# Performance work log

Hardware: AMD Instinct MI355X
Metric: run time of the kernel (lower is better)

The kernel has to match this reference:

```python
import jax, jax.numpy as jnp
import numpy as np


def setup_inputs() -> dict:
    key = jax.random.key(0)
    # coeffs_tensor: stacked/padded wavelet coefficients [B, F, T]
    coeffs = jax.random.normal(key, (16, 256, 8192), dtype=jnp.float32)
    return {"coeffs": coeffs}


def reference(coeffs) -> jnp.ndarray:
    B, F, T = coeffs.shape
    # torch.angle on a real tensor -> 0 for x>=0, pi for x<0; jnp.angle matches.
    phase = jnp.angle(coeffs)
    inst_freq = jnp.diff(phase, axis=-1)
    inst_freq = jnp.pad(inst_freq, ((0, 0), (0, 0), (0, 1)))  # F.pad(..., (0,1))
    freq_adjusted = jnp.clip(inst_freq, -1.0, 1.0)  # [B,F,T]
    # k = (f + freq_adjusted).long(); .long() truncates toward zero, as does astype(int32)
    f_idx = jnp.arange(F, dtype=coeffs.dtype)[None, :, None]
    k = jnp.clip((f_idx + freq_adjusted).astype(jnp.int32), 0, F - 1)  # [B,F,T]
    # Fused scatter-add over all (b, f, t): sst[b, k[b,f,t], t] += coeffs[b, f, t]
    b_idx = jnp.arange(B)[:, None, None]
    t_idx = jnp.arange(T)[None, None, :]
    sst = jnp.zeros_like(coeffs).at[b_idx, k, t_idx].add(coeffs)
    return sst
```

## Files before the change

kernel.cpp:

```cpp
#include <hip/hip_runtime.h>

typedef float f32x4 __attribute__((ext_vector_type(4)));

#define BB 16
#define FF 256
#define TT 8192
#define F_CHUNK 8
#define ROWS (F_CHUNK + 2)
#define THREADS 256

__device__ __forceinline__ int sgn_bit(float x) {
    return (int)(__float_as_uint(x) >> 31);
}

__global__ __launch_bounds__(THREADS, 6) void sst_kernel(const float* __restrict__ in,
                                                         float* __restrict__ out) {
    const int t  = blockIdx.x * (THREADS * 4) + threadIdx.x * 4;
    const int fs = blockIdx.y * F_CHUNK;
    const int b  = blockIdx.z;

    const float* src = in  + (size_t)b * FF * TT + t;
    float*       dst = out + (size_t)b * FF * TT + t;

    const bool tail = (t + 4 >= TT);
    const int  eoff = tail ? 3 : 4;

    f32x4    v[ROWS];
    float    e[ROWS];
    unsigned pk[ROWS];

    #pragma unroll
    for (int i = 0; i < ROWS; ++i) {
        int f = fs - 1 + i;
        f = f < 0 ? 0 : (f > FF - 1 ? FF - 1 : f);
        const float* p = src + (size_t)f * TT;
        v[i] = *reinterpret_cast<const f32x4*>(p);
        e[i] = p[eoff];
    }

    __builtin_amdgcn_sched_barrier(0);

    #pragma unroll
    for (int i = 0; i < ROWS; ++i) {
        const int f = fs - 1 + i;
        const bool oob = (f < 0) | (f > FF - 1);
        const int s0 = sgn_bit(v[i][0]), s1 = sgn_bit(v[i][1]),
                  s2 = sgn_bit(v[i][2]), s3 = sgn_bit(v[i][3]), s4 = sgn_bit(e[i]);
        const int a0 = s1 - s0 + 1;
        const int a1 = s2 - s1 + 1;
        const int a2 = s3 - s2 + 1;
        const int a3 = tail ? 1 : (s4 - s3 + 1);
        pk[i] = oob ? 0x55u : (unsigned)(a0 | (a1 << 2) | (a2 << 4) | (a3 << 6));
    }

    #pragma unroll
    for (int i = 1; i <= F_CHUNK; ++i) {
        const int g = fs + (i - 1);
        const bool isFirst = (g == 0);
        const bool isLast  = (g == FF - 1);

        const unsigned pp = pk[i - 1], pc = pk[i], pn = pk[i + 1];
        const f32x4    vp = v[i - 1],  vc = v[i],  vn = v[i + 1];

        f32x4 r;
        {
            const unsigned cp = pp & 3u, cc = pc & 3u, cn = pn & 3u;
            const bool bc = (cc == 1u) || (isFirst && cc == 0u) || (isLast && cc == 2u);
            r[0] = ((cp == 2u) ? vp[0] : 0.f) + (bc ? vc[0] : 0.f) + ((cn == 0u) ? vn[0] : 0.f);
        }
        {
            const unsigned cp = (pp >> 2) & 3u, cc = (pc >> 2) & 3u, cn = (pn >> 2) & 3u;
            const bool bc = (cc == 1u) || (isFirst && cc == 0u) || (isLast && cc == 2u);
            r[1] = ((cp == 2u) ? vp[1] : 0.f) + (bc ? vc[1] : 0.f) + ((cn == 0u) ? vn[1] : 0.f);
        }
        {
            const unsigned cp = (pp >> 4) & 3u, cc = (pc >> 4) & 3u, cn = (pn >> 4) & 3u;
            const bool bc = (cc == 1u) || (isFirst && cc == 0u) || (isLast && cc == 2u);
            r[2] = ((cp == 2u) ? vp[2] : 0.f) + (bc ? vc[2] : 0.f) + ((cn == 0u) ? vn[2] : 0.f);
        }
        {
            const unsigned cp = (pp >> 6) & 3u, cc = (pc >> 6) & 3u, cn = (pn >> 6) & 3u;
            const bool bc = (cc == 1u) || (isFirst && cc == 0u) || (isLast && cc == 2u);
            r[3] = ((cp == 2u) ? vp[3] : 0.f) + (bc ? vc[3] : 0.f) + ((cn == 0u) ? vn[3] : 0.f);
        }

        __builtin_nontemporal_store(r, reinterpret_cast<f32x4*>(dst + (size_t)g * TT));
    }
}

extern "C" void kernel_launch(void* const* d_in, const int* in_sizes, int n_in,
                              void* d_out, int out_size, void* d_ws, size_t ws_size,
                              hipStream_t stream) {
    const float* in  = (const float*)d_in[0];
    float*       out = (float*)d_out;
    dim3 grid(TT / (THREADS * 4), FF / F_CHUNK, BB);
    sst_kernel<<<grid, THREADS, 0, stream>>>(in, out);
}
```

Before: 236.7 us.

## Loop over time tiles per block with double-buffered global-to-LDS async loads

Each block now owns an F-chunk for one batch and walks all time tiles, staging rows into LDS through global_load_lds DMA with two buffers so the next tiles load while the current one computes. Tile-boundary columns, whose next element lies in the following tile, are patched in a separate epilogue that rereads global memory. This is meant to hide load latency and remove the per-block extra edge loads. The cost is far fewer blocks (512) that each run long, hand-tuned vmcnt counts that must exactly match the DMA ordering, and an epilogue with scattered scalar accesses.

```diff
diff --git a/kernel.cpp b/kernel.cpp
--- a/kernel.cpp
+++ b/kernel.cpp
@@ -8,83 +8,150 @@
 #define F_CHUNK 8
 #define ROWS (F_CHUNK + 2)
 #define THREADS 256
+#define TBLK (THREADS * 4)
+#define TILES (TT / TBLK)
+#define LROW 1024
+
+__device__ __forceinline__ void dma16(const float* g, float* l) {
+    __builtin_amdgcn_global_load_lds(
+        (const __attribute__((address_space(1))) unsigned int*)g,
+        (__attribute__((address_space(3))) unsigned int*)l,
+        16, 0, 0);
+}
 
 __device__ __forceinline__ int sgn_bit(float x) {
     return (int)(__float_as_uint(x) >> 31);
 }
 
-__global__ __launch_bounds__(THREADS, 6) void sst_kernel(const float* __restrict__ in,
-                                                         float* __restrict__ out) {
-    const int t  = blockIdx.x * (THREADS * 4) + threadIdx.x * 4;
-    const int fs = blockIdx.y * F_CHUNK;
-    const int b  = blockIdx.z;
+__global__ __launch_bounds__(THREADS) void sst_kernel(const float* __restrict__ in,
+                                                      float* __restrict__ out) {
+    __shared__ float sm[2][ROWS][LROW];
 
-    const float* src = in  + (size_t)b * FF * TT + t;
-    float*       dst = out + (size_t)b * FF * TT + t;
+    const int tid  = threadIdx.x;
+    const int wid  = tid >> 6;
+    const int tid4 = tid * 4;
+    const int fs   = blockIdx.x * F_CHUNK;
+    const int b    = blockIdx.y;
 
-    const bool tail = (t + 4 >= TT);
-    const int  eoff = tail ? 3 : 4;
+    const float* srcR = in  + (size_t)b * FF * TT;
+    float*       dstR = out + (size_t)b * FF * TT;
 
-    f32x4    v[ROWS];
-    float    e[ROWS];
-    unsigned pk[ROWS];
+    const int eidx = (tid4 + 4 > LROW - 1) ? (LROW - 1) : (tid4 + 4);
+
+#define STAGE(tt, bb_) do {                                                        \
+        _Pragma("unroll")                                                          \
+        for (int i_ = 0; i_ < ROWS; ++i_) {                                        \
+            int f_ = fs - 1 + i_;                                                  \
+            f_ = f_ < 0 ? 0 : (f_ > FF - 1 ? FF - 1 : f_);                         \
+            dma16(srcR + (size_t)f_ * TT + (tt) * TBLK + tid4,                     \
+                  &sm[bb_][i_][wid * 256]);                                        \
+        }                                                                          \
+    } while (0)
+
+    STAGE(0, 0);
+    STAGE(1, 1);
 
     #pragma unroll
-    for (int i = 0; i < ROWS; ++i) {
-        int f = fs - 1 + i;
-        f = f < 0 ? 0 : (f > FF - 1 ? FF - 1 : f);
-        const float* p = src + (size_t)f * TT;
-        v[i] = *reinterpret_cast<const f32x4*>(p);
-        e[i] = p[eoff];
-    }
+    for (int k = 0; k < TILES; ++k) {
+        if (k == 0)              asm volatile("s_waitcnt vmcnt(10)" ::: "memory");
+        else if (k == TILES - 1) asm volatile("s_waitcnt vmcnt(16)" ::: "memory");
+        else                     asm volatile("s_waitcnt vmcnt(18)" ::: "memory");
+        __builtin_amdgcn_sched_barrier(0);
+        __builtin_amdgcn_s_barrier();
+        asm volatile("" ::: "memory");
 
-    __builtin_amdgcn_sched_barrier(0);
+        const int bb = k & 1;
 
-    #pragma unroll
-    for (int i = 0; i < ROWS; ++i) {
-        const int f = fs - 1 + i;
-        const bool oob = (f < 0) | (f > FF - 1);
-        const int s0 = sgn_bit(v[i][0]), s1 = sgn_bit(v[i][1]),
-                  s2 = sgn_bit(v[i][2]), s3 = sgn_bit(v[i][3]), s4 = sgn_bit(e[i]);
-        const int a0 = s1 - s0 + 1;
-        const int a1 = s2 - s1 + 1;
-        const int a2 = s3 - s2 + 1;
-        const int a3 = tail ? 1 : (s4 - s3 + 1);
-        pk[i] = oob ? 0x55u : (unsigned)(a0 | (a1 << 2) | (a2 << 4) | (a3 << 6));
-    }
+        f32x4 v[ROWS];
+        float ee[ROWS];
+        #pragma unroll
+        for (int i = 0; i < ROWS; ++i) {
+            v[i]  = *reinterpret_cast<const f32x4*>(&sm[bb][i][tid4]);
+            ee[i] = sm[bb][i][eidx];
+        }
+        asm volatile("s_waitcnt lgkmcnt(0)" ::: "memory");
+        __builtin_amdgcn_sched_barrier(0);
+        __builtin_amdgcn_s_barrier();
+        asm volatile("" ::: "memory");
 
-    #pragma unroll
-    for (int i = 1; i <= F_CHUNK; ++i) {
-        const int g = fs + (i - 1);
-        const bool isFirst = (g == 0);
-        const bool isLast  = (g == FF - 1);
+        if (k + 2 < TILES) STAGE(k + 2, bb);
 
-        const unsigned pp = pk[i - 1], pc = pk[i], pn = pk[i + 1];
-        const f32x4    vp = v[i - 1],  vc = v[i],  vn = v[i + 1];
-
-        f32x4 r;
-        {
-            const unsigned cp = pp & 3u, cc = pc & 3u, cn = pn & 3u;
-            const bool bc = (cc == 1u) || (isFirst && cc == 0u) || (isLast && cc == 2u);
-            r[0] = ((cp == 2u) ? vp[0] : 0.f) + (bc ? vc[0] : 0.f) + ((cn == 0u) ? vn[0] : 0.f);
-        }
-        {
-            const unsigned cp = (pp >> 2) & 3u, cc = (pc >> 2) & 3u, cn = (pn >> 2) & 3u;
-            const bool bc = (cc == 1u) || (isFirst && cc == 0u) || (isLast && cc == 2u);
-            r[1] = ((cp == 2u) ? vp[1] : 0.f) + (bc ? vc[1] : 0.f) + ((cn == 0u) ? vn[1] : 0.f);
-        }
-        {
-            const unsigned cp = (pp >> 4) & 3u, cc = (pc >> 4) & 3u, cn = (pn >> 4) & 3u;
-            const bool bc = (cc == 1u) || (isFirst && cc == 0u) || (isLast && cc == 2u);
-            r[2] = ((cp == 2u) ? vp[2] : 0.f) + (bc ? vc[2] : 0.f) + ((cn == 0u) ? vn[2] : 0.f);
-        }
-        {
-            const unsigned cp = (pp >> 6) & 3u, cc = (pc >> 6) & 3u, cn = (pn >> 6) & 3u;
-            const bool bc = (cc == 1u) || (isFirst && cc == 0u) || (isLast && cc == 2u);
-            r[3] = ((cp == 2u) ? vp[3] : 0.f) + (bc ? vc[3] : 0.f) + ((cn == 0u) ? vn[3] : 0.f);
+        const bool tail = (k == TILES - 1) && (tid == THREADS - 1);
+        unsigned pk[ROWS];
+        #pragma unroll
+        for (int i = 0; i < ROWS; ++i) {
+            const int f = fs - 1 + i;
+            const bool oob = (f < 0) | (f > FF - 1);
+            const int s0 = sgn_bit(v[i][0]), s1 = sgn_bit(v[i][1]),
+                      s2 = sgn_bit(v[i][2]), s3 = sgn_bit(v[i][3]), s4 = sgn_bit(ee[i]);
+            const int a0 = s1 - s0 + 1;
+            const int a1 = s2 - s1 + 1;
+            const int a2 = s3 - s2 + 1;
+            const int a3 = tail ? 1 : (s4 - s3 + 1);
+            pk[i] = oob ? 0x55u : (unsigned)(a0 | (a1 << 2) | (a2 << 4) | (a3 << 6));
         }
 
-        __builtin_nontemporal_store(r, reinterpret_cast<f32x4*>(dst + (size_t)g * TT));
+        #pragma unroll
+        for (int i = 1; i <= F_CHUNK; ++i) {
+            const int g = fs + (i - 1);
+            const bool isFirst = (g == 0);
+            const bool isLast  = (g == FF - 1);
+
+            const unsigned pp = pk[i - 1], pc = pk[i], pn = pk[i + 1];
+            const f32x4    vp = v[i - 1],  vc = v[i],  vn = v[i + 1];
+
+            f32x4 r;
+            {
+                const unsigned cp = pp & 3u, cc = pc & 3u, cn = pn & 3u;
+                const bool bc = (cc == 1u) || (isFirst && cc == 0u) || (isLast && cc == 2u);
+                r[0] = ((cp == 2u) ? vp[0] : 0.f) + (bc ? vc[0] : 0.f) + ((cn == 0u) ? vn[0] : 0.f);
+            }
+            {
+                const unsigned cp = (pp >> 2) & 3u, cc = (pc >> 2) & 3u, cn = (pn >> 2) & 3u;
+                const bool bc = (cc == 1u) || (isFirst && cc == 0u) || (isLast && cc == 2u);
+                r[1] = ((cp == 2u) ? vp[1] : 0.f) + (bc ? vc[1] : 0.f) + ((cn == 0u) ? vn[1] : 0.f);
+            }
+            {
+                const unsigned cp = (pp >> 4) & 3u, cc = (pc >> 4) & 3u, cn = (pn >> 4) & 3u;
+                const bool bc = (cc == 1u) || (isFirst && cc == 0u) || (isLast && cc == 2u);
+                r[2] = ((cp == 2u) ? vp[2] : 0.f) + (bc ? vc[2] : 0.f) + ((cn == 0u) ? vn[2] : 0.f);
+            }
+            {
+                const unsigned cp = (pp >> 6) & 3u, cc = (pc >> 6) & 3u, cn = (pn >> 6) & 3u;
+                const bool bc = (cc == 1u) || (isFirst && cc == 0u) || (isLast && cc == 2u);
+                r[3] = ((cp == 2u) ? vp[3] : 0.f) + (bc ? vc[3] : 0.f) + ((cn == 0u) ? vn[3] : 0.f);
+            }
+
+            __builtin_nontemporal_store(
+                r, reinterpret_cast<f32x4*>(dstR + (size_t)g * TT + k * TBLK + tid4));
+        }
+    }
+#undef STAGE
+
+    asm volatile("s_waitcnt vmcnt(0)" ::: "memory");
+    __builtin_amdgcn_sched_barrier(0);
+    __builtin_amdgcn_s_barrier();
+    asm volatile("" ::: "memory");
+
+    if (tid < (TILES - 1) * F_CHUNK) {
+        const int kb = tid >> 3;
+        const int j  = tid & 7;
+        const int g  = fs + j;
+        const int c  = kb * TBLK + (TBLK - 1);
+
+        auto S = [&](int f, int cc) -> int {
+            return sgn_bit(srcR[(size_t)f * TT + cc]);
+        };
+        const int am = (g - 1 >= 0)     ? (S(g - 1, c + 1) - S(g - 1, c)) : 9;
+        const int ac =                     S(g,     c + 1) - S(g,     c);
+        const int an = (g + 1 <= FF - 1) ? (S(g + 1, c + 1) - S(g + 1, c)) : 9;
+        const bool bc = (ac == 0) || (g == 0 && ac < 0) || (g == FF - 1 && ac > 0);
+
+        float r = 0.f;
+        if (am == 1)  r += srcR[(size_t)(g - 1) * TT + c];
+        if (bc)       r += srcR[(size_t)g * TT + c];
+        if (an == -1) r += srcR[(size_t)(g + 1) * TT + c];
+        dstR[(size_t)g * TT + c] = r;
     }
 }
 
@@ -93,6 +160,6 @@
                               hipStream_t stream) {
     const float* in  = (const float*)d_in[0];
     float*       out = (float*)d_out;
-    dim3 grid(TT / (THREADS * 4), FF / F_CHUNK, BB);
+    dim3 grid(FF / F_CHUNK, BB);
     sst_kernel<<<grid, THREADS, 0, stream>>>(in, out);
 }
```

Measured after the change: 247.3 us. 4.5% more time.
